# Kernel optimization log

Measured on AMD Instinct MI355X. Metric: run time of the kernel, lower is better.

The kernel has to match this reference:

```python
import jax, jax.numpy as jnp
import numpy as np
import math

B, S, D = 4, 128, 2560
H, HD = 32, 80
FFN = 10240
DEC, ENC = 256, 256
EPS = 1e-5


def setup_inputs() -> dict:
    key = jax.random.key(0)
    ks = iter(jax.random.split(key, 40))

    def w(shape, scale=0.02):
        return jax.random.normal(next(ks), shape, jnp.float32) * scale

    inp = {}
    inp["x"] = jax.random.normal(next(ks), (B, S, D), jnp.float32)
    inp["xa"] = jax.random.normal(next(ks), (B, S, D), jnp.float32)
    # self-attn mask: causal over the S prefill positions, False on unfilled cache tail
    j = jnp.arange(DEC)
    i = jnp.arange(S)
    m = (j[None, :] <= i[:, None]) & (j[None, :] < S)  # [S, DEC]
    inp["mask"] = jnp.broadcast_to(m[None, None], (B, 1, S, DEC))
    inp["cross_mask"] = jnp.broadcast_to((jnp.arange(ENC) < S)[None, None, None], (B, 1, 1, ENC))
    # LayerNorms
    for n in ["ln1", "ln2", "ln3"]:
        inp[n + "_g"] = jnp.ones((D,), jnp.float32)
        inp[n + "_b"] = jnp.zeros((D,), jnp.float32)
    # self-attn projections ([in, out] layout for x @ W)
    for p in ["sa", "ca"]:
        for n in ["wq", "wk", "wv", "wo"]:
            inp[p + "_" + n] = w((D, D))
        for n in ["bq", "bk", "bv", "bo"]:
            inp[p + "_" + n] = jnp.zeros((D,), jnp.float32)
    inp["cache_sk"] = jnp.zeros((B, H, DEC, HD), jnp.float32)
    inp["cache_sv"] = jnp.zeros((B, H, DEC, HD), jnp.float32)
    inp["cache_ck"] = jnp.zeros((B, H, ENC, HD), jnp.float32)
    inp["cache_cv"] = jnp.zeros((B, H, ENC, HD), jnp.float32)
    inp["fc1_w"] = w((D, FFN))
    inp["fc1_b"] = jnp.zeros((FFN,), jnp.float32)
    inp["fc2_w"] = w((FFN, D))
    inp["fc2_b"] = jnp.zeros((D,), jnp.float32)
    return inp


def _ln(h, g, b):
    h32 = h.astype(jnp.float32)
    mu = h32.mean(-1, keepdims=True)
    var = ((h32 - mu) ** 2).mean(-1, keepdims=True)
    return ((h32 - mu) * jax.lax.rsqrt(var + EPS) * g + b).astype(h.dtype)


def _heads(t):
    b, s, _ = t.shape
    return t.reshape(b, s, H, HD).transpose(0, 2, 1, 3)  # [B,H,S,HD]


def _attn(q, k_cache, v_cache, mask):
    kf = k_cache.astype(q.dtype)
    vf = v_cache.astype(q.dtype)
    scores = jnp.einsum("bhqd,bhkd->bhqk", q, kf) / math.sqrt(HD)
    if mask is not None:
        scores = jnp.where(mask, scores, jnp.finfo(scores.dtype).min)
    attn = jax.nn.softmax(scores.astype(jnp.float32), axis=-1).astype(q.dtype)
    o = jnp.einsum("bhqk,bhkd->bhqd", attn, vf)
    b, h, s, hd = o.shape
    return o.transpose(0, 2, 1, 3).reshape(b, s, h * hd)


def reference(x, xa, mask, cross_mask,
              ln1_g, ln1_b, sa_wq, sa_bq, sa_wk, sa_bk, sa_wv, sa_bv, sa_wo, sa_bo,
              cache_sk, cache_sv,
              ln2_g, ln2_b, ca_wq, ca_bq, ca_wk, ca_bk, ca_wv, ca_bv, ca_wo, ca_bo,
              cache_ck, cache_cv,
              ln3_g, ln3_b, fc1_w, fc1_b, fc2_w, fc2_b):
    # --- self-attention (prefill path: scatter with arange indices = prefix write) ---
    h = _ln(x, ln1_g, ln1_b)
    q = _heads(h @ sa_wq + sa_bq)
    k = _heads(h @ sa_wk + sa_bk)
    v = _heads(h @ sa_wv + sa_bv)
    s = q.shape[2]
    sk = cache_sk.at[:, :, :s, :].set(k.astype(jnp.float32))
    sv = cache_sv.at[:, :, :s, :].set(v.astype(jnp.float32))
    o = _attn(q, sk, sv, mask)
    x = x + (o @ sa_wo + sa_bo)

    # --- cross-attention: K/V from encoder output, scattered into cache ---
    h = _ln(x, ln2_g, ln2_b)
    q = _heads(h @ ca_wq + ca_bq)
    k = _heads(xa @ ca_wk + ca_bk)
    v = _heads(xa @ ca_wv + ca_bv)
    kv = k.shape[2]
    ck = cache_ck.at[:, :, :kv, :].set(k.astype(jnp.float32))
    cv = cache_cv.at[:, :, :kv, :].set(v.astype(jnp.float32))
    o = _attn(q, ck, cv, cross_mask)
    x = x + (o @ ca_wo + ca_bo)

    # --- MLP: fc1 -> GELU (exact) -> fc2 ---
    h = _ln(x, ln3_g, ln3_b)
    x = x + (jax.nn.gelu(h @ fc1_w + fc1_b, approximate=False) @ fc2_w + fc2_b)
    return (x, sk, sv, ck, cv)
```

## Files before the change

### kernel.cpp

```cpp
#include <hip/hip_runtime.h>
#include <hip/hip_bf16.h>
#include <math.h>

#define TB   4
#define TS   128
#define TD   2560
#define TH   32
#define THD  80
#define TFFN 10240
#define TDEC 256
#define TM   (TB * TS)
#define CACHE_N ((size_t)TB * TH * TDEC * THD)

using short8  = __attribute__((ext_vector_type(8))) short;
using floatx4 = __attribute__((ext_vector_type(4))) float;

__device__ __forceinline__ short f2bf(float f) {
  unsigned u = __builtin_bit_cast(unsigned, f);
  u += 0x7fff + ((u >> 16) & 1);
  return (short)(u >> 16);
}
__device__ __forceinline__ float bf2f(short s) {
  unsigned u = ((unsigned)(unsigned short)s) << 16;
  return __builtin_bit_cast(float, u);
}

enum { EPI_PLAIN = 0, EPI_GELU = 2, EPI_SCATTER = 3 };

struct GArgs {
  const short* A[3];
  const float* B[3];
  const float* bias[3];
  float*       outf[3];
  short*       outb[3];
  int          mode[3];
  int tilesPerSeg;
  int N;
  int lda;
  int Kc;
};

__device__ __forceinline__ void stage_load(const short* __restrict__ A,
                                           const float* __restrict__ B,
                                           int lda, int N, int m0, int n0, int k0,
                                           int tid, short8 ra[2], float rb[16])
{
  const int cb = (tid & 3) * 8;
  const int rr = tid >> 2;
#pragma unroll
  for (int it = 0; it < 2; ++it)
    ra[it] = *(const short8*)(A + (size_t)(m0 + rr + it * 64) * lda + k0 + cb);
  const int n  = tid & 127;
  const int kg = (tid >> 7) * 16;
  const float* bp = B + (size_t)(k0 + kg) * N + n0 + n;
#pragma unroll
  for (int j = 0; j < 16; ++j)
    rb[j] = bp[(size_t)j * N];
}

__device__ __forceinline__ void stage_commit(short* __restrict__ As, short* __restrict__ Bs,
                                             int tid, const short8 ra[2], const float rb[16])
{
  const int cb = (tid & 3) * 8;
  const int rr = tid >> 2;
#pragma unroll
  for (int it = 0; it < 2; ++it)
    *(short8*)(&As[(rr + it * 64) * 40 + cb]) = ra[it];
  const int n  = tid & 127;
  const int kg = (tid >> 7) * 16;
  short8 lo, hi;
#pragma unroll
  for (int j = 0; j < 8; ++j) { lo[j] = f2bf(rb[j]); hi[j] = f2bf(rb[8 + j]); }
  *(short8*)(&Bs[n * 40 + kg])     = lo;
  *(short8*)(&Bs[n * 40 + kg + 8]) = hi;
}

__global__ __launch_bounds__(256, 2)
void gemmF(GArgs g)
{
  __shared__ short As[2][128 * 40];
  __shared__ short Bs[2][128 * 40];

  const int seg = blockIdx.x / g.tilesPerSeg;
  const int tx  = blockIdx.x % g.tilesPerSeg;
  const short* A = g.A[seg];
  const float* B = g.B[seg];
  const int N = g.N, lda = g.lda;
  const int m0 = blockIdx.y * 128;
  const int n0 = tx * 128;
  const int z  = blockIdx.z;
  const int k0base = z * g.Kc;
  const int nk = g.Kc / 32;

  const int tid = threadIdx.x;
  const int lane = tid & 63;
  const int wv = tid >> 6;
  const int wm = (wv >> 1) * 64;
  const int wn = (wv & 1) * 64;
  const int lr = lane & 15;
  const int lq = lane >> 4;

  floatx4 acc[4][4];
#pragma unroll
  for (int i = 0; i < 4; ++i)
#pragma unroll
    for (int j = 0; j < 4; ++j)
      acc[i][j] = floatx4{0.f, 0.f, 0.f, 0.f};

  short8 ra[2]; float rb[16];
  stage_load(A, B, lda, N, m0, n0, k0base, tid, ra, rb);
  stage_commit(As[0], Bs[0], tid, ra, rb);
  __syncthreads();

  for (int ki = 0; ki < nk; ++ki) {
    const int cur = ki & 1;
    const bool more = (ki + 1 < nk);
    if (more)
      stage_load(A, B, lda, N, m0, n0, k0base + (ki + 1) * 32, tid, ra, rb);

    short8 af[4], bfr[4];
#pragma unroll
    for (int t = 0; t < 4; ++t)
      af[t] = *(const short8*)(&As[cur][(wm + t * 16 + lr) * 40 + lq * 8]);
#pragma unroll
    for (int t = 0; t < 4; ++t)
      bfr[t] = *(const short8*)(&Bs[cur][(wn + t * 16 + lr) * 40 + lq * 8]);
#pragma unroll
    for (int tm = 0; tm < 4; ++tm)
#pragma unroll
      for (int tn = 0; tn < 4; ++tn)
        acc[tm][tn] = __builtin_amdgcn_mfma_f32_16x16x32_bf16(af[tm], bfr[tn],
                                                              acc[tm][tn], 0, 0, 0);
    if (more)
      stage_commit(As[cur ^ 1], Bs[cur ^ 1], tid, ra, rb);
    __syncthreads();
  }

  const float* bias = g.bias[seg];
  float* outf = g.outf[seg];
  short* outb = g.outb[seg];
  const int mode = g.mode[seg];
#pragma unroll
  for (int tm = 0; tm < 4; ++tm) {
#pragma unroll
    for (int tn = 0; tn < 4; ++tn) {
      const int col = n0 + wn + tn * 16 + lr;
      const float bv = bias ? bias[col] : 0.f;
      int hh = 0, hd = 0;
      if (mode == EPI_SCATTER) { hh = col / THD; hd = col % THD; }
#pragma unroll
      for (int r = 0; r < 4; ++r) {
        const int row = m0 + wm + tm * 16 + lq * 4 + r;
        float v = acc[tm][tn][r] + bv;
        if (mode == EPI_PLAIN) {
          outf[(size_t)z * TM * N + (size_t)row * N + col] = v;
        } else if (mode == EPI_GELU) {
          float gg = 0.5f * v * (1.0f + erff(v * 0.70710678118654752f));
          outb[(size_t)row * N + col] = f2bf(gg);
        } else {
          int b = row >> 7, s = row & 127;
          outf[(((size_t)b * TH + hh) * TDEC + s) * THD + hd] = v;
        }
      }
    }
  }
}

template<bool CAUSAL>
__global__ __launch_bounds__(256, 2)
void attn_kernel(const float* __restrict__ q, const float* __restrict__ kc,
                 const float* __restrict__ vc, short* __restrict__ ob)
{
  __shared__ short kb[TS * THD];
  __shared__ short vb[TS * THD];
  __shared__ float qf[64 * 84];
  short* pb = (short*)qf;

  const int tid = threadIdx.x;
  const int bh = blockIdx.x;
  const int b = bh >> 5, h = bh & 31;
  const int r0 = blockIdx.y * 64;

  const size_t cbase = (size_t)bh * TDEC * THD;
  for (int idx = tid; idx < TS * THD; idx += 256) {
    kb[idx] = f2bf(kc[cbase + idx]);
    vb[idx] = f2bf(vc[cbase + idx]);
  }
  for (int idx = tid; idx < 64 * THD; idx += 256) {
    int r = idx / THD, d = idx - r * THD;
    qf[r * 84 + d] = q[(size_t)(b * TS + r0 + r) * TD + h * THD + d];
  }
  __syncthreads();

  const int r = tid >> 2;
  const int quarter = tid & 3;
  const int qi = r0 + r;

  float sc[32];
#pragma unroll 1
  for (int jj = 0; jj < 32; ++jj) {
    int j = quarter + jj * 4;
    if (CAUSAL && j > qi) { sc[jj] = -1e30f; continue; }
    float a = 0.f;
#pragma unroll 8
    for (int d = 0; d < THD; ++d)
      a += qf[r * 84 + d] * bf2f(kb[j * THD + d]);
    sc[jj] = a * 0.11180339887498949f;
  }

  float mx = -1e30f;
#pragma unroll
  for (int jj = 0; jj < 32; ++jj) mx = fmaxf(mx, sc[jj]);
  mx = fmaxf(mx, __shfl_xor(mx, 1));
  mx = fmaxf(mx, __shfl_xor(mx, 2));
  float sum = 0.f;
#pragma unroll
  for (int jj = 0; jj < 32; ++jj) { sc[jj] = __expf(sc[jj] - mx); sum += sc[jj]; }
  sum += __shfl_xor(sum, 1);
  sum += __shfl_xor(sum, 2);
  const float rinv = 1.0f / sum;

  __syncthreads();
#pragma unroll
  for (int jj = 0; jj < 32; ++jj)
    pb[r * TS + quarter + jj * 4] = f2bf(sc[jj] * rinv);
  __syncthreads();

  for (int it = 0; it < 20; ++it) {
    int idx = tid + it * 256;
    int rr = idx / THD, d = idx - rr * THD;
    float a = 0.f;
#pragma unroll 8
    for (int j = 0; j < TS; ++j)
      a += bf2f(pb[rr * TS + j]) * bf2f(vb[j * THD + d]);
    ob[(size_t)(b * TS + r0 + rr) * TD + h * THD + d] = f2bf(a);
  }
}

__global__ __launch_bounds__(256, 4)
void ln_kernel(const float* __restrict__ x, const float* __restrict__ g,
               const float* __restrict__ bb, short* __restrict__ out)
{
  const int row = blockIdx.x;
  const float* xr = x + (size_t)row * TD;
  const int tid = threadIdx.x;
  float vals[10];
  float s = 0.f, ss = 0.f;
#pragma unroll
  for (int it = 0; it < 10; ++it) {
    float v = xr[tid + it * 256];
    vals[it] = v; s += v; ss += v * v;
  }
#pragma unroll
  for (int o = 32; o > 0; o >>= 1) { s += __shfl_xor(s, o); ss += __shfl_xor(ss, o); }
  __shared__ float red[8];
  const int wv = tid >> 6, lane = tid & 63;
  if (lane == 0) { red[wv] = s; red[wv + 4] = ss; }
  __syncthreads();
  s  = red[0] + red[1] + red[2] + red[3];
  ss = red[4] + red[5] + red[6] + red[7];
  const float mu = s * (1.0f / TD);
  const float rstd = rsqrtf(ss * (1.0f / TD) - mu * mu + 1e-5f);
  short* orow = out + (size_t)row * TD;
#pragma unroll
  for (int it = 0; it < 10; ++it) {
    int i = tid + it * 256;
    orow[i] = f2bf((vals[it] - mu) * rstd * g[i] + bb[i]);
  }
}

__global__ __launch_bounds__(256, 4)
void ln_fuse_kernel(const float* __restrict__ xin, const float* __restrict__ p,
                    const float* __restrict__ obias,
                    const float* __restrict__ g, const float* __restrict__ bb,
                    short* __restrict__ hout, float* __restrict__ xout)
{
  const int row = blockIdx.x;
  const int tid = threadIdx.x;
  const size_t base = (size_t)row * TD;
  const float* p0 = p;
  const float* p1 = p + (size_t)TM * TD;
  float vals[10];
  float s = 0.f, ss = 0.f;
#pragma unroll
  for (int it = 0; it < 10; ++it) {
    int i = tid + it * 256;
    float v = xin[base + i] + p0[base + i] + p1[base + i] + obias[i];
    vals[it] = v; xout[base + i] = v; s += v; ss += v * v;
  }
#pragma unroll
  for (int o = 32; o > 0; o >>= 1) { s += __shfl_xor(s, o); ss += __shfl_xor(ss, o); }
  __shared__ float red[8];
  const int wv = tid >> 6, lane = tid & 63;
  if (lane == 0) { red[wv] = s; red[wv + 4] = ss; }
  __syncthreads();
  s  = red[0] + red[1] + red[2] + red[3];
  ss = red[4] + red[5] + red[6] + red[7];
  const float mu = s * (1.0f / TD);
  const float rstd = rsqrtf(ss * (1.0f / TD) - mu * mu + 1e-5f);
#pragma unroll
  for (int it = 0; it < 10; ++it) {
    int i = tid + it * 256;
    hout[base + i] = f2bf((vals[it] - mu) * rstd * g[i] + bb[i]);
  }
}

__global__ void fc2_combine_kernel(const float* __restrict__ x2, const float* __restrict__ p,
                                   const float* __restrict__ bias, float* __restrict__ out)
{
  const size_t i = (size_t)blockIdx.x * 256 + threadIdx.x;
  const int col = (int)(i % TD);
  const size_t S1 = (size_t)TM * TD;
  out[i] = x2[i] + p[i] + p[i + S1] + p[i + 2 * S1] + p[i + 3 * S1] + bias[col];
}

__global__ void cvt_bf16_kernel(const float* __restrict__ in, short* __restrict__ out, int n)
{
  int i = blockIdx.x * 256 + threadIdx.x;
  if (i < n) out[i] = f2bf(in[i]);
}

__global__ void tailcopy_kernel(const float* __restrict__ src, float* __restrict__ dst)
{
  int off4 = blockIdx.x * 256 + threadIdx.x;
  int chunk = blockIdx.y;
  size_t pos = (size_t)chunk * 5120 + 2560 + off4;
  ((float4*)dst)[pos] = ((const float4*)src)[pos];
}

extern "C" void kernel_launch(void* const* d_in, const int* in_sizes, int n_in,
                              void* d_out, int out_size, void* d_ws, size_t ws_size,
                              hipStream_t stream)
{
  (void)in_sizes; (void)n_in; (void)out_size; (void)ws_size;
  const float* x        = (const float*)d_in[0];
  const float* xa       = (const float*)d_in[1];
  const float* ln1_g    = (const float*)d_in[4];
  const float* ln1_b    = (const float*)d_in[5];
  const float* ln2_g    = (const float*)d_in[6];
  const float* ln2_b    = (const float*)d_in[7];
  const float* ln3_g    = (const float*)d_in[8];
  const float* ln3_b    = (const float*)d_in[9];
  const float* sa_wq    = (const float*)d_in[10];
  const float* sa_wk    = (const float*)d_in[11];
  const float* sa_wv    = (const float*)d_in[12];
  const float* sa_wo    = (const float*)d_in[13];
  const float* sa_bq    = (const float*)d_in[14];
  const float* sa_bk    = (const float*)d_in[15];
  const float* sa_bv    = (const float*)d_in[16];
  const float* sa_bo    = (const float*)d_in[17];
  const float* ca_wq    = (const float*)d_in[18];
  const float* ca_wk    = (const float*)d_in[19];
  const float* ca_wv    = (const float*)d_in[20];
  const float* ca_wo    = (const float*)d_in[21];
  const float* ca_bq    = (const float*)d_in[22];
  const float* ca_bk    = (const float*)d_in[23];
  const float* ca_bv    = (const float*)d_in[24];
  const float* ca_bo    = (const float*)d_in[25];
  const float* cache_sk = (const float*)d_in[26];
  const float* cache_sv = (const float*)d_in[27];
  const float* cache_ck = (const float*)d_in[28];
  const float* cache_cv = (const float*)d_in[29];
  const float* fc1_w    = (const float*)d_in[30];
  const float* fc1_b    = (const float*)d_in[31];
  const float* fc2_w    = (const float*)d_in[32];
  const float* fc2_b    = (const float*)d_in[33];

  float* out_x  = (float*)d_out;
  float* out_sk = out_x + (size_t)TM * TD;
  float* out_sv = out_sk + CACHE_N;
  float* out_ck = out_sv + CACHE_N;
  float* out_cv = out_ck + CACHE_N;

  char* w = (char*)d_ws;
  short* h_b   = (short*)w; w += (size_t)TM * TD * 2;
  short* xa_b  = (short*)w; w += (size_t)TM * TD * 2;
  short* o_b   = (short*)w; w += (size_t)TM * TD * 2;
  short* ffn_b = (short*)w; w += (size_t)TM * TFFN * 2;
  float* qbuf  = (float*)w; w += (size_t)TM * TD * 4;
  float* x1    = (float*)w; w += (size_t)TM * TD * 4;
  float* x2    = (float*)w; w += (size_t)TM * TD * 4;
  float* pbuf  = (float*)w; w += (size_t)TM * TD * 4 * 4;

  const dim3 blk(256);
  const dim3 gAttn(TB * TH, 2);

  cvt_bf16_kernel<<<dim3(TM * TD / 256), blk, 0, stream>>>(xa, xa_b, TM * TD);
  tailcopy_kernel<<<dim3(10, TB * TH), blk, 0, stream>>>(cache_sk, out_sk);
  tailcopy_kernel<<<dim3(10, TB * TH), blk, 0, stream>>>(cache_sv, out_sv);
  tailcopy_kernel<<<dim3(10, TB * TH), blk, 0, stream>>>(cache_ck, out_ck);
  tailcopy_kernel<<<dim3(10, TB * TH), blk, 0, stream>>>(cache_cv, out_cv);

  ln_kernel<<<dim3(TM), blk, 0, stream>>>(x, ln1_g, ln1_b, h_b);
  {
    GArgs a{};
    a.A[0] = h_b;  a.B[0] = sa_wq; a.bias[0] = sa_bq; a.outf[0] = qbuf;   a.mode[0] = EPI_PLAIN;
    a.A[1] = h_b;  a.B[1] = sa_wk; a.bias[1] = sa_bk; a.outf[1] = out_sk; a.mode[1] = EPI_SCATTER;
    a.A[2] = h_b;  a.B[2] = sa_wv; a.bias[2] = sa_bv; a.outf[2] = out_sv; a.mode[2] = EPI_SCATTER;
    a.tilesPerSeg = 20; a.N = TD; a.lda = TD; a.Kc = TD;
    gemmF<<<dim3(60, 4, 1), blk, 0, stream>>>(a);
  }
  attn_kernel<true><<<gAttn, blk, 0, stream>>>(qbuf, out_sk, out_sv, o_b);
  {
    GArgs a{};
    a.A[0] = o_b; a.B[0] = sa_wo; a.bias[0] = nullptr; a.outf[0] = pbuf; a.mode[0] = EPI_PLAIN;
    a.tilesPerSeg = 20; a.N = TD; a.lda = TD; a.Kc = TD / 2;
    gemmF<<<dim3(20, 4, 2), blk, 0, stream>>>(a);
  }
  ln_fuse_kernel<<<dim3(TM), blk, 0, stream>>>(x, pbuf, sa_bo, ln2_g, ln2_b, h_b, x1);

  {
    GArgs a{};
    a.A[0] = h_b;  a.B[0] = ca_wq; a.bias[0] = ca_bq; a.outf[0] = qbuf;   a.mode[0] = EPI_PLAIN;
    a.A[1] = xa_b; a.B[1] = ca_wk; a.bias[1] = ca_bk; a.outf[1] = out_ck; a.mode[1] = EPI_SCATTER;
    a.A[2] = xa_b; a.B[2] = ca_wv; a.bias[2] = ca_bv; a.outf[2] = out_cv; a.mode[2] = EPI_SCATTER;
    a.tilesPerSeg = 20; a.N = TD; a.lda = TD; a.Kc = TD;
    gemmF<<<dim3(60, 4, 1), blk, 0, stream>>>(a);
  }
  attn_kernel<false><<<gAttn, blk, 0, stream>>>(qbuf, out_ck, out_cv, o_b);
  {
    GArgs a{};
    a.A[0] = o_b; a.B[0] = ca_wo; a.bias[0] = nullptr; a.outf[0] = pbuf; a.mode[0] = EPI_PLAIN;
    a.tilesPerSeg = 20; a.N = TD; a.lda = TD; a.Kc = TD / 2;
    gemmF<<<dim3(20, 4, 2), blk, 0, stream>>>(a);
  }
  ln_fuse_kernel<<<dim3(TM), blk, 0, stream>>>(x1, pbuf, ca_bo, ln3_g, ln3_b, h_b, x2);

  {
    GArgs a{};
    a.A[0] = h_b; a.B[0] = fc1_w; a.bias[0] = fc1_b; a.outb[0] = ffn_b; a.mode[0] = EPI_GELU;
    a.tilesPerSeg = 80; a.N = TFFN; a.lda = TD; a.Kc = TD;
    gemmF<<<dim3(80, 4, 1), blk, 0, stream>>>(a);
  }
  {
    GArgs a{};
    a.A[0] = ffn_b; a.B[0] = fc2_w; a.bias[0] = nullptr; a.outf[0] = pbuf; a.mode[0] = EPI_PLAIN;
    a.tilesPerSeg = 20; a.N = TD; a.lda = TFFN; a.Kc = TFFN / 4;
    gemmF<<<dim3(20, 4, 4), blk, 0, stream>>>(a);
  }
  fc2_combine_kernel<<<dim3(TM * TD / 256), blk, 0, stream>>>(x2, pbuf, fc2_b, out_x);
}
```

Measured before the change: 1.001 ms.

## Split-K all GEMMs more deeply and move epilogues into separate reduction kernels

Every GEMM now uses split-K (4-way for QKV, 8-way for the output projections and fc2, 2-way for fc1), writing fp32 partials to a larger scratch buffer. Bias add, GELU and the KV-cache scatter move out of the GEMM epilogue into new vectorized combine kernels. The goal is to fill more CUs, since the weight-streaming GEMMs with M=512 launch few tiles. The cost is much more fp32 partial traffic (fc1 alone writes two 512x10240 fp32 partials) plus extra kernel launches.

```diff
diff --git a/kernel.cpp b/kernel.cpp
--- a/kernel.cpp
+++ b/kernel.cpp
@@ -13,6 +13,7 @@
 #define CACHE_N ((size_t)TB * TH * TDEC * THD)
 
 using short8  = __attribute__((ext_vector_type(8))) short;
+using sshort4 = __attribute__((ext_vector_type(4))) short;
 using floatx4 = __attribute__((ext_vector_type(4))) float;
 
 __device__ __forceinline__ short f2bf(float f) {
@@ -25,15 +26,10 @@
   return __builtin_bit_cast(float, u);
 }
 
-enum { EPI_PLAIN = 0, EPI_GELU = 2, EPI_SCATTER = 3 };
-
 struct GArgs {
   const short* A[3];
   const float* B[3];
-  const float* bias[3];
   float*       outf[3];
-  short*       outb[3];
-  int          mode[3];
   int tilesPerSeg;
   int N;
   int lda;
@@ -136,34 +132,80 @@
     __syncthreads();
   }
 
-  const float* bias = g.bias[seg];
   float* outf = g.outf[seg];
-  short* outb = g.outb[seg];
-  const int mode = g.mode[seg];
 #pragma unroll
   for (int tm = 0; tm < 4; ++tm) {
 #pragma unroll
     for (int tn = 0; tn < 4; ++tn) {
       const int col = n0 + wn + tn * 16 + lr;
-      const float bv = bias ? bias[col] : 0.f;
-      int hh = 0, hd = 0;
-      if (mode == EPI_SCATTER) { hh = col / THD; hd = col % THD; }
 #pragma unroll
       for (int r = 0; r < 4; ++r) {
         const int row = m0 + wm + tm * 16 + lq * 4 + r;
-        float v = acc[tm][tn][r] + bv;
-        if (mode == EPI_PLAIN) {
-          outf[(size_t)z * TM * N + (size_t)row * N + col] = v;
-        } else if (mode == EPI_GELU) {
-          float gg = 0.5f * v * (1.0f + erff(v * 0.70710678118654752f));
-          outb[(size_t)row * N + col] = f2bf(gg);
-        } else {
-          int b = row >> 7, s = row & 127;
-          outf[(((size_t)b * TH + hh) * TDEC + s) * THD + hd] = v;
-        }
+        outf[(size_t)z * TM * N + (size_t)row * N + col] = acc[tm][tn][r];
       }
     }
   }
+}
+
+template<int Z>
+__global__ void qkv_combine_kernel(const float* __restrict__ p,
+                                   const float* __restrict__ bq,
+                                   const float* __restrict__ bk,
+                                   const float* __restrict__ bv,
+                                   float* __restrict__ qbuf,
+                                   float* __restrict__ sk,
+                                   float* __restrict__ sv)
+{
+  const int i4 = blockIdx.x * 256 + threadIdx.x;
+  const int row = i4 / 1920;
+  const int c4  = i4 - row * 1920;
+  const int col = c4 * 4;
+  const int seg = (col >= 2 * TD) ? 2 : (col >= TD ? 1 : 0);
+  const int c   = col - seg * TD;
+  const float* base = p + (size_t)seg * ((size_t)Z * TM * TD) + (size_t)row * TD + c;
+  float4 v = *(const float4*)base;
+#pragma unroll
+  for (int zz = 1; zz < Z; ++zz) {
+    float4 t = *(const float4*)(base + (size_t)zz * TM * TD);
+    v.x += t.x; v.y += t.y; v.z += t.z; v.w += t.w;
+  }
+  const float* bias = (seg == 0) ? bq : (seg == 1 ? bk : bv);
+  float4 b4 = *(const float4*)(bias + c);
+  v.x += b4.x; v.y += b4.y; v.z += b4.z; v.w += b4.w;
+  if (seg == 0) {
+    *(float4*)(qbuf + (size_t)row * TD + c) = v;
+  } else {
+    const int hh = c / THD, hd = c % THD;
+    const int b = row >> 7, sI = row & 127;
+    float* dst = (seg == 1) ? sk : sv;
+    *(float4*)(dst + (((size_t)(b * TH + hh) * TDEC + sI) * THD + hd)) = v;
+  }
+}
+
+template<int Z>
+__global__ void fc1_gelu_kernel(const float* __restrict__ p,
+                                const float* __restrict__ bias,
+                                short* __restrict__ out)
+{
+  const int i4 = blockIdx.x * 256 + threadIdx.x;
+  const int row = i4 / (TFFN / 4);
+  const int c4  = i4 - row * (TFFN / 4);
+  const int col = c4 * 4;
+  const size_t idx = (size_t)row * TFFN + col;
+  float4 v = *(const float4*)(p + idx);
+#pragma unroll
+  for (int zz = 1; zz < Z; ++zz) {
+    float4 t = *(const float4*)(p + (size_t)zz * TM * TFFN + idx);
+    v.x += t.x; v.y += t.y; v.z += t.z; v.w += t.w;
+  }
+  float4 b4 = *(const float4*)(bias + col);
+  v.x += b4.x; v.y += b4.y; v.z += b4.z; v.w += b4.w;
+  sshort4 o;
+  o[0] = f2bf(0.5f * v.x * (1.0f + erff(v.x * 0.70710678118654752f)));
+  o[1] = f2bf(0.5f * v.y * (1.0f + erff(v.y * 0.70710678118654752f)));
+  o[2] = f2bf(0.5f * v.z * (1.0f + erff(v.z * 0.70710678118654752f)));
+  o[3] = f2bf(0.5f * v.w * (1.0f + erff(v.w * 0.70710678118654752f)));
+  *(sshort4*)(out + idx) = o;
 }
 
 template<bool CAUSAL>
@@ -269,6 +311,7 @@
   }
 }
 
+template<int Z>
 __global__ __launch_bounds__(256, 4)
 void ln_fuse_kernel(const float* __restrict__ xin, const float* __restrict__ p,
                     const float* __restrict__ obias,
@@ -278,14 +321,15 @@
   const int row = blockIdx.x;
   const int tid = threadIdx.x;
   const size_t base = (size_t)row * TD;
-  const float* p0 = p;
-  const float* p1 = p + (size_t)TM * TD;
   float vals[10];
   float s = 0.f, ss = 0.f;
 #pragma unroll
   for (int it = 0; it < 10; ++it) {
     int i = tid + it * 256;
-    float v = xin[base + i] + p0[base + i] + p1[base + i] + obias[i];
+    float v = xin[base + i] + obias[i];
+#pragma unroll
+    for (int zz = 0; zz < Z; ++zz)
+      v += p[(size_t)zz * TM * TD + base + i];
     vals[it] = v; xout[base + i] = v; s += v; ss += v * v;
   }
 #pragma unroll
@@ -305,13 +349,21 @@
   }
 }
 
+template<int Z>
 __global__ void fc2_combine_kernel(const float* __restrict__ x2, const float* __restrict__ p,
                                    const float* __restrict__ bias, float* __restrict__ out)
 {
-  const size_t i = (size_t)blockIdx.x * 256 + threadIdx.x;
+  const size_t i = ((size_t)blockIdx.x * 256 + threadIdx.x) * 4;
   const int col = (int)(i % TD);
-  const size_t S1 = (size_t)TM * TD;
-  out[i] = x2[i] + p[i] + p[i + S1] + p[i + 2 * S1] + p[i + 3 * S1] + bias[col];
+  float4 v = *(const float4*)(x2 + i);
+#pragma unroll
+  for (int zz = 0; zz < Z; ++zz) {
+    float4 t = *(const float4*)(p + (size_t)zz * TM * TD + i);
+    v.x += t.x; v.y += t.y; v.z += t.z; v.w += t.w;
+  }
+  float4 b4 = *(const float4*)(bias + col);
+  v.x += b4.x; v.y += b4.y; v.z += b4.z; v.w += b4.w;
+  *(float4*)(out + i) = v;
 }
 
 __global__ void cvt_bf16_kernel(const float* __restrict__ in, short* __restrict__ out, int n)
@@ -380,7 +432,7 @@
   float* qbuf  = (float*)w; w += (size_t)TM * TD * 4;
   float* x1    = (float*)w; w += (size_t)TM * TD * 4;
   float* x2    = (float*)w; w += (size_t)TM * TD * 4;
-  float* pbuf  = (float*)w; w += (size_t)TM * TD * 4 * 4;
+  float* pbuf  = (float*)w; w += (size_t)TM * TD * 4 * 12;
 
   const dim3 blk(256);
   const dim3 gAttn(TB * TH, 2);
@@ -394,49 +446,54 @@
   ln_kernel<<<dim3(TM), blk, 0, stream>>>(x, ln1_g, ln1_b, h_b);
   {
     GArgs a{};
-    a.A[0] = h_b;  a.B[0] = sa_wq; a.bias[0] = sa_bq; a.outf[0] = qbuf;   a.mode[0] = EPI_PLAIN;
-    a.A[1] = h_b;  a.B[1] = sa_wk; a.bias[1] = sa_bk; a.outf[1] = out_sk; a.mode[1] = EPI_SCATTER;
-    a.A[2] = h_b;  a.B[2] = sa_wv; a.bias[2] = sa_bv; a.outf[2] = out_sv; a.mode[2] = EPI_SCATTER;
-    a.tilesPerSeg = 20; a.N = TD; a.lda = TD; a.Kc = TD;
-    gemmF<<<dim3(60, 4, 1), blk, 0, stream>>>(a);
-  }
+    a.A[0] = h_b; a.B[0] = sa_wq; a.outf[0] = pbuf;
+    a.A[1] = h_b; a.B[1] = sa_wk; a.outf[1] = pbuf + (size_t)4 * TM * TD;
+    a.A[2] = h_b; a.B[2] = sa_wv; a.outf[2] = pbuf + (size_t)8 * TM * TD;
+    a.tilesPerSeg = 20; a.N = TD; a.lda = TD; a.Kc = TD / 4;
+    gemmF<<<dim3(60, 4, 4), blk, 0, stream>>>(a);
+  }
+  qkv_combine_kernel<4><<<dim3(TM * 7680 / 4 / 256), blk, 0, stream>>>(
+      pbuf, sa_bq, sa_bk, sa_bv, qbuf, out_sk, out_sv);
   attn_kernel<true><<<gAttn, blk, 0, stream>>>(qbuf, out_sk, out_sv, o_b);
   {
     GArgs a{};
-    a.A[0] = o_b; a.B[0] = sa_wo; a.bias[0] = nullptr; a.outf[0] = pbuf; a.mode[0] = EPI_PLAIN;
-    a.tilesPerSeg = 20; a.N = TD; a.lda = TD; a.Kc = TD / 2;
-    gemmF<<<dim3(20, 4, 2), blk, 0, stream>>>(a);
-  }
-  ln_fuse_kernel<<<dim3(TM), blk, 0, stream>>>(x, pbuf, sa_bo, ln2_g, ln2_b, h_b, x1);
-
-  {
-    GArgs a{};
-    a.A[0] = h_b;  a.B[0] = ca_wq; a.bias[0] = ca_bq; a.outf[0] = qbuf;   a.mode[0] = EPI_PLAIN;
-    a.A[1] = xa_b; a.B[1] = ca_wk; a.bias[1] = ca_bk; a.outf[1] = out_ck; a.mode[1] = EPI_SCATTER;
-    a.A[2] = xa_b; a.B[2] = ca_wv; a.bias[2] = ca_bv; a.outf[2] = out_cv; a.mode[2] = EPI_SCATTER;
-    a.tilesPerSeg = 20; a.N = TD; a.lda = TD; a.Kc = TD;
-    gemmF<<<dim3(60, 4, 1), blk, 0, stream>>>(a);
-  }
+    a.A[0] = o_b; a.B[0] = sa_wo; a.outf[0] = pbuf;
+    a.tilesPerSeg = 20; a.N = TD; a.lda = TD; a.Kc = TD / 8;
+    gemmF<<<dim3(20, 4, 8), blk, 0, stream>>>(a);
+  }
+  ln_fuse_kernel<8><<<dim3(TM), blk, 0, stream>>>(x, pbuf, sa_bo, ln2_g, ln2_b, h_b, x1);
+
+  {
+    GArgs a{};
+    a.A[0] = h_b;  a.B[0] = ca_wq; a.outf[0] = pbuf;
+    a.A[1] = xa_b; a.B[1] = ca_wk; a.outf[1] = pbuf + (size_t)4 * TM * TD;
+    a.A[2] = xa_b; a.B[2] = ca_wv; a.outf[2] = pbuf + (size_t)8 * TM * TD;
+    a.tilesPerSeg = 20; a.N = TD; a.lda = TD; a.Kc = TD / 4;
+    gemmF<<<dim3(60, 4, 4), blk, 0, stream>>>(a);
+  }
+  qkv_combine_kernel<4><<<dim3(TM * 7680 / 4 / 256), blk, 0, stream>>>(
+      pbuf, ca_bq, ca_bk, ca_bv, qbuf, out_ck, out_cv);
   attn_kernel<false><<<gAttn, blk, 0, stream>>>(qbuf, out_ck, out_cv, o_b);
   {
     GArgs a{};
-    a.A[0] = o_b; a.B[0] = ca_wo; a.bias[0] = nullptr; a.outf[0] = pbuf; a.mode[0] = EPI_PLAIN;
-    a.tilesPerSeg = 20; a.N = TD; a.lda = TD; a.Kc = TD / 2;
-    gemmF<<<dim3(20, 4, 2), blk, 0, stream>>>(a);
-  }
-  ln_fuse_kernel<<<dim3(TM), blk, 0, stream>>>(x1, pbuf, ca_bo, ln3_g, ln3_b, h_b, x2);
-
-  {
-    GArgs a{};
-    a.A[0] = h_b; a.B[0] = fc1_w; a.bias[0] = fc1_b; a.outb[0] = ffn_b; a.mode[0] = EPI_GELU;
-    a.tilesPerSeg = 80; a.N = TFFN; a.lda = TD; a.Kc = TD;
-    gemmF<<<dim3(80, 4, 1), blk, 0, stream>>>(a);
-  }
-  {
-    GArgs a{};
-    a.A[0] = ffn_b; a.B[0] = fc2_w; a.bias[0] = nullptr; a.outf[0] = pbuf; a.mode[0] = EPI_PLAIN;
-    a.tilesPerSeg = 20; a.N = TD; a.lda = TFFN; a.Kc = TFFN / 4;
-    gemmF<<<dim3(20, 4, 4), blk, 0, stream>>>(a);
-  }
-  fc2_combine_kernel<<<dim3(TM * TD / 256), blk, 0, stream>>>(x2, pbuf, fc2_b, out_x);
-}
+    a.A[0] = o_b; a.B[0] = ca_wo; a.outf[0] = pbuf;
+    a.tilesPerSeg = 20; a.N = TD; a.lda = TD; a.Kc = TD / 8;
+    gemmF<<<dim3(20, 4, 8), blk, 0, stream>>>(a);
+  }
+  ln_fuse_kernel<8><<<dim3(TM), blk, 0, stream>>>(x1, pbuf, ca_bo, ln3_g, ln3_b, h_b, x2);
+
+  {
+    GArgs a{};
+    a.A[0] = h_b; a.B[0] = fc1_w; a.outf[0] = pbuf;
+    a.tilesPerSeg = 80; a.N = TFFN; a.lda = TD; a.Kc = TD / 2;
+    gemmF<<<dim3(80, 4, 2), blk, 0, stream>>>(a);
+  }
+  fc1_gelu_kernel<2><<<dim3(TM * TFFN / 4 / 256), blk, 0, stream>>>(pbuf, fc1_b, ffn_b);
+  {
+    GArgs a{};
+    a.A[0] = ffn_b; a.B[0] = fc2_w; a.outf[0] = pbuf;
+    a.tilesPerSeg = 20; a.N = TD; a.lda = TFFN; a.Kc = TFFN / 8;
+    gemmF<<<dim3(20, 4, 8), blk, 0, stream>>>(a);
+  }
+  fc2_combine_kernel<8><<<dim3(TM * TD / 4 / 256), blk, 0, stream>>>(x2, pbuf, fc2_b, out_x);
+}
```

New measurement: 893.1 us. -10.8%, faster.
